# Kernel optimization log

Hardware: AMD Instinct MI355X
Metric: run time of the kernel (lower is better)

## Reference

```python
import jax, jax.numpy as jnp
import numpy as np

LRU_DIM = 256
HIDDEN = 256
H = 64
N = LRU_DIM // H  # 4 (even, per assert)
R_MIN, R_MAX, MAX_PHASE = 0.9, 0.999, 6.28
BSZ, T = 8, 4096


def _rotate_half(x):
    # interleaved pairs: [x0,x1,x2,x3,...] -> [-x1,x0,-x3,x2,...]
    r = jnp.stack([-x[..., 1::2], x[..., 0::2]], axis=-1)
    return r.reshape(x.shape)


def _mix_sequence(gamma, thetas, Us):
    # gamma: scalar, thetas: (N/2,), Us: (T,B,N) -> (T,B,N)
    Tlen = Us.shape[0]
    gammas = jnp.broadcast_to(gamma, (Tlen,))
    ths = jnp.broadcast_to(thetas, (Tlen,) + thetas.shape)

    def binf(a, b):
        gi, ti, xi = a
        gj, tj, xj = b
        theta = jnp.repeat(tj, 2, axis=-1)            # (T, N): [t0,t0,t1,t1,...]
        sin = jnp.sin(theta)[..., None, :]            # (T,1,N)
        cos = jnp.cos(theta)[..., None, :]
        acc = gj[..., None, None] * (cos * xi + sin * _rotate_half(xi)) + xj
        return (gi * gj, ti + tj, acc)

    _, _, res = jax.lax.associative_scan(binf, (gammas, ths, Us), axis=0)
    return res


def setup_inputs() -> dict:
    key = jax.random.key(0)
    ks = jax.random.split(key, 7)
    scale = 1.0 / np.sqrt(HIDDEN + LRU_DIM)
    u = jax.random.normal(ks[0], (BSZ, HIDDEN, T), dtype=jnp.float32)
    thetas_log = jnp.log(jax.random.uniform(ks[1], (H, N // 2), minval=0.01, maxval=1.0) * MAX_PHASE).astype(jnp.float32)
    P_param = (jax.random.normal(ks[2], (H, N, N), dtype=jnp.float32) / np.sqrt(LRU_DIM + N)).astype(jnp.float32)
    B_param = (jax.random.normal(ks[3], (H, N, HIDDEN), dtype=jnp.float32) * scale).astype(jnp.float32)
    C = (jax.random.normal(ks[4], (HIDDEN, LRU_DIM), dtype=jnp.float32) * scale).astype(jnp.float32)
    D = jax.random.normal(ks[5], (HIDDEN,), dtype=jnp.float32)
    u1 = jax.random.uniform(ks[6], (H,))
    gamma_log = (np.log(-np.log(R_MAX)) + u1 * (np.log(-np.log(R_MIN)) - np.log(-np.log(R_MAX)))).astype(jnp.float32)
    return {"u": u, "thetas_log": thetas_log, "P_param": P_param,
            "B_param": B_param, "C": C, "D": D, "gamma_log": gamma_log}


def reference(u, thetas_log, P_param, B_param, C, D, gamma_log):
    Bsz, hidden, Tlen = u.shape
    ut = jnp.transpose(u, (0, 2, 1))                       # (B,T,Dh)
    gamma = jnp.exp(-jnp.exp(gamma_log))                   # (H,)
    trace_per_head = jnp.sum(B_param * B_param, axis=(1, 2))  # tr(B B^T) per head
    norm = jnp.sqrt((1.0 - gamma ** 2) / trace_per_head)
    B_norm = norm[:, None, None] * B_param                 # (H,N,Dh)
    skew = P_param - jnp.swapaxes(P_param, 1, 2)
    P = jax.vmap(jax.scipy.linalg.expm)(skew)              # (H,N,N), orthogonal
    Us = jnp.einsum('HnD,BTD->HTBn', B_norm, ut)           # (H,T,B,N)
    Us = jnp.einsum('HNn,HTBn->HTBN', P, Us)               # == einsum with P^T as in torch
    thetas = jnp.exp(thetas_log)                           # (H,N/2)
    y = jax.vmap(_mix_sequence)(gamma, thetas, Us)         # (H,T,B,N)
    y = jnp.einsum('HNn,HTBN->HTBn', P, y)
    y = jnp.transpose(y, (2, 1, 0, 3)).reshape(Bsz, Tlen, -1)  # (B,T,lru_dim)
    y = jnp.einsum('Dn,BTn->BTD', C, y) + D * ut
    return jnp.transpose(y, (0, 2, 1))                     # (B,Dh,T)
```

## Files before the change

kernel.cpp:

```cpp
#include <hip/hip_runtime.h>
#include <hip/hip_bf16.h>
#include <math.h>


typedef __attribute__((ext_vector_type(8))) short short8;
typedef __attribute__((ext_vector_type(4))) float f32x4;

#define TLEN 4096
#define LCH 64
#define NCH 64
#define BSZ 8
#define LDK 264
#define LDW 132

constexpr int MB_OFF   = 0;
constexpr int CB_OFF   = 32768;
constexpr int AP_OFF   = 65536;
constexpr int ALP_OFF  = AP_OFF + 65 * 256;
constexpr int TOT_OFF  = ALP_OFF + 65 * 256;
constexpr int PL_OFF   = TOT_OFF + NCH * BSZ * 256;
constexpr int NORM_OFF = PL_OFF + 1024;
constexpr int S_OFF    = NORM_OFF + 64;

__device__ __forceinline__ float bfbits2f(unsigned int bits16) {
  union { unsigned int u; float f; } v; v.u = bits16 << 16; return v.f;
}
__device__ __forceinline__ unsigned int f2bfbits(float f) {
  union { float f; unsigned int u; } v; v.f = f;
  return (v.u + 0x7fffu + ((v.u >> 16) & 1u)) >> 16;
}
__device__ __forceinline__ unsigned int pack2(float x, float y) {
  return f2bfbits(x) | (f2bfbits(y) << 16);
}

__global__ __launch_bounds__(256) void k0a_precompute(
    const float* __restrict__ thetas_log, const float* __restrict__ P_param,
    const float* __restrict__ B_param, const float* __restrict__ gamma_log,
    float* __restrict__ ws) {
  __shared__ float tracep[64][4];
  __shared__ double gamma_d[64];
  const int tid = threadIdx.x;
  {
    int h = tid >> 2, q = tid & 3;
    const float* bp = B_param + (h * 4 + q) * 256;
    float s = 0.f;
    for (int i = 0; i < 256; ++i) { float v = bp[i]; s += v * v; }
    tracep[h][q] = s;
  }
  __syncthreads();
  if (tid < 64) {
    int h = tid;
    double g = exp(-exp((double)gamma_log[h]));
    gamma_d[h] = g;
    double tr = (double)tracep[h][0] + tracep[h][1] + tracep[h][2] + tracep[h][3];
    ws[NORM_OFF + h] = (float)sqrt((1.0 - g * g) / tr);
    double A[4][4], E[4][4], Tm[4][4];
    for (int i = 0; i < 4; ++i)
      for (int j = 0; j < 4; ++j)
        A[i][j] = (double)P_param[h * 16 + i * 4 + j] - (double)P_param[h * 16 + j * 4 + i];
    double fro = 0.0;
    for (int i = 0; i < 4; ++i) for (int j = 0; j < 4; ++j) fro += A[i][j] * A[i][j];
    fro = sqrt(fro);
    int s = 0;
    while (fro > 0.25 && s < 30) { fro *= 0.5; ++s; }
    double scl = 1.0;
    for (int q2 = 0; q2 < s; ++q2) scl *= 0.5;
    for (int i = 0; i < 4; ++i) for (int j = 0; j < 4; ++j) A[i][j] *= scl;
    for (int i = 0; i < 4; ++i)
      for (int j = 0; j < 4; ++j) { E[i][j] = (i == j) ? 1.0 : 0.0; Tm[i][j] = E[i][j]; }
    for (int k = 1; k <= 16; ++k) {
      double Tn[4][4];
      for (int i = 0; i < 4; ++i)
        for (int j = 0; j < 4; ++j) {
          double acc = 0.0;
          for (int m = 0; m < 4; ++m) acc += Tm[i][m] * A[m][j];
          Tn[i][j] = acc / (double)k;
        }
      for (int i = 0; i < 4; ++i)
        for (int j = 0; j < 4; ++j) { Tm[i][j] = Tn[i][j]; E[i][j] += Tn[i][j]; }
    }
    for (int q2 = 0; q2 < s; ++q2) {
      double E2[4][4];
      for (int i = 0; i < 4; ++i)
        for (int j = 0; j < 4; ++j) {
          double acc = 0.0;
          for (int m = 0; m < 4; ++m) acc += E[i][m] * E[m][j];
          E2[i][j] = acc;
        }
      for (int i = 0; i < 4; ++i) for (int j = 0; j < 4; ++j) E[i][j] = E2[i][j];
    }
    for (int i = 0; i < 4; ++i)
      for (int j = 0; j < 4; ++j) ws[PL_OFF + h * 16 + i * 4 + j] = (float)E[i][j];
  }
  __syncthreads();
  if (tid < 128) {
    int h = tid >> 1, p = tid & 1;
    double th = exp((double)thetas_log[h * 2 + p]);
    double g = gamma_d[h];
    double ar = g * cos(th), ai = g * sin(th);
    float2* Apw = (float2*)(ws + AP_OFF);
    float2* ALp = (float2*)(ws + ALP_OFF);
    double xr = 1.0, xi = 0.0;
    Apw[tid] = make_float2(1.f, 0.f);
    for (int j = 1; j <= LCH; ++j) {
      double nr = xr * ar - xi * ai, ni = xr * ai + xi * ar;
      xr = nr; xi = ni;
      Apw[j * 128 + tid] = make_float2((float)xr, (float)xi);
    }
    double br = xr, bi = xi;
    xr = 1.0; xi = 0.0;
    ALp[tid] = make_float2(1.f, 0.f);
    for (int k = 1; k <= NCH; ++k) {
      double nr = xr * br - xi * bi, ni = xr * bi + xi * br;
      xr = nr; xi = ni;
      ALp[k * 128 + tid] = make_float2((float)xr, (float)xi);
    }
  }
}

__global__ __launch_bounds__(256) void k0b_mats(
    const float* __restrict__ B_param, const float* __restrict__ C,
    float* __restrict__ ws) {
  const float* Pl  = ws + PL_OFF;
  const float* nrm = ws + NORM_OFF;
  unsigned short* Mbf = (unsigned short*)(ws + MB_OFF);
  unsigned short* Cbf = (unsigned short*)(ws + CB_OFF);
  const int blk = blockIdx.x, tid = threadIdx.x;
  if (blk < 16) {
    for (int rr = 0; rr < 16; ++rr) {
      int r = blk * 16 + rr, h = r >> 2, N = r & 3;
      float acc = 0.f;
      for (int n = 0; n < 4; ++n)
        acc += Pl[h * 16 + N * 4 + n] * B_param[(h * 4 + n) * 256 + tid];
      Mbf[r * 256 + tid] = (unsigned short)f2bfbits(nrm[h] * acc);
    }
  } else {
    int h = tid >> 2;
    int N = tid & 3;
    for (int rr = 0; rr < 16; ++rr) {
      int Do = (blk - 16) * 16 + rr;
      float acc = 0.f;
      for (int n = 0; n < 4; ++n)
        acc += C[Do * 256 + (tid & ~3) + n] * Pl[h * 16 + N * 4 + n];
      Cbf[Do * 256 + tid] = (unsigned short)f2bfbits(acc);
    }
  }
}

__global__ __launch_bounds__(256) void k1_mfma(
    const float* __restrict__ u, float* __restrict__ ws) {
  __shared__ __align__(16) unsigned char smem[64 * LDK * 2];
  unsigned short* us = (unsigned short*)smem;
  unsigned int*   wd = (unsigned int*)smem;

  const int c = blockIdx.x, b = blockIdx.y;
  const int t0 = c * LCH;
  const int tid = threadIdx.x;
  const int L = tid & 63;
  const int w = __builtin_amdgcn_readfirstlane(tid >> 6);
  const int qh = L >> 4, l15 = L & 15;

  {
    const int kbase = tid >> 4;
    const int t4 = (tid & 15) * 4;
#pragma unroll
    for (int i = 0; i < 16; ++i) {
      int d = kbase + i * 16;
      float4 v = *(const float4*)(u + (size_t)(b * 256 + d) * TLEN + t0 + t4);
      float vv[4] = {v.x, v.y, v.z, v.w};
#pragma unroll
      for (int dt = 0; dt < 4; ++dt) {
        int t = t4 + dt;
        us[t * LDK + (d ^ ((t & 3) << 3))] = (unsigned short)f2bfbits(vv[dt]);
      }
    }
  }
  __syncthreads();

  f32x4 acc[4][4];
#pragma unroll
  for (int rt = 0; rt < 4; ++rt)
#pragma unroll
    for (int tt = 0; tt < 4; ++tt) acc[rt][tt] = (f32x4){0.f, 0.f, 0.f, 0.f};
  {
    const unsigned short* Mbf = (const unsigned short*)(ws + MB_OFF);
#pragma unroll
    for (int ks = 0; ks < 8; ++ks) {
      short8 af[4], bf[4];
#pragma unroll
      for (int rt = 0; rt < 4; ++rt)
        af[rt] = *(const short8*)(Mbf + (size_t)(w * 64 + rt * 16 + l15) * 256 + ks * 32 + qh * 8);
#pragma unroll
      for (int tt = 0; tt < 4; ++tt) {
        int row = tt * 16 + l15;
        int col = (ks * 32 + qh * 8) ^ ((row & 3) << 3);
        bf[tt] = *(const short8*)(us + row * LDK + col);
      }
#pragma unroll
      for (int rt = 0; rt < 4; ++rt)
#pragma unroll
        for (int tt = 0; tt < 4; ++tt)
          acc[rt][tt] = __builtin_amdgcn_mfma_f32_16x16x32_bf16(af[rt], bf[tt], acc[rt][tt], 0, 0, 0);
    }
  }
  __syncthreads();

#pragma unroll
  for (int rt = 0; rt < 4; ++rt) {
    int pbase = w * 32 + rt * 8 + qh * 2;
#pragma unroll
    for (int tt = 0; tt < 4; ++tt) {
      int t = tt * 16 + l15;
      f32x4 a4 = acc[rt][tt];
      wd[t * LDW + pbase]     = pack2(a4[0], a4[1]);
      wd[t * LDW + pbase + 1] = pack2(a4[2], a4[3]);
    }
  }
  __syncthreads();

  if (tid < 128) {
    const int p = tid;
    const float2* Apw = (const float2*)(ws + AP_OFF);
    float2 a = Apw[128 + p];
    float zr = 0.f, zi = 0.f;
#pragma unroll
    for (int t = 0; t < LCH; ++t) {
      unsigned int wv = wd[t * LDW + p];
      float wr = bfbits2f(wv & 0xffffu), wi = bfbits2f(wv >> 16);
      float nr = fmaf(a.x, zr, fmaf(-a.y, zi, wr));
      float ni = fmaf(a.x, zi, fmaf(a.y, zr, wi));
      zr = nr; zi = ni;
      wd[t * LDW + p] = pack2(zr, zi);
    }
    ((float2*)(ws + TOT_OFF))[(c * BSZ + b) * 128 + p] = make_float2(zr, zi);
  }
  __syncthreads();

  unsigned int* Sg = (unsigned int*)(ws + S_OFF);
#pragma unroll
  for (int i = 0; i < 32; ++i) {
    int idx = tid + 256 * i;
    int t = idx >> 7, q = idx & 127;
    Sg[(size_t)(t0 + t) * 1024 + b * 128 + q] = wd[t * LDW + q];
  }
}

__global__ __launch_bounds__(256) void k3_mfma(
    const float* __restrict__ u, const float* __restrict__ Dv,
    const float* __restrict__ ws, float* __restrict__ out) {
  __shared__ __align__(16) unsigned char smem[64 * LDK * 2];
  unsigned int* zd = (unsigned int*)smem;

  const int c = blockIdx.x, b = blockIdx.y;
  const int t0 = c * LCH;
  const int tid = threadIdx.x;
  const int L = tid & 63;
  const int w = __builtin_amdgcn_readfirstlane(tid >> 6);
  const int qh = L >> 4, l15 = L & 15;
  const unsigned int* Sg = (const unsigned int*)(ws + S_OFF);

  if (tid < 128) {
    const int p = tid;
    float cr = 0.f, ci = 0.f;
    const float2* ALp = (const float2*)(ws + ALP_OFF);
    const float2* Tot = (const float2*)(ws + TOT_OFF);
    for (int cp = 0; cp < c; ++cp) {
      float2 al = ALp[(c - 1 - cp) * 128 + p];
      float2 tv = Tot[(cp * BSZ + b) * 128 + p];
      cr = fmaf(al.x, tv.x, fmaf(-al.y, tv.y, cr));
      ci = fmaf(al.x, tv.y, fmaf(al.y, tv.x, ci));
    }
    const float2* Apw = (const float2*)(ws + AP_OFF);
#pragma unroll
    for (int t = 0; t < LCH; ++t) {
      unsigned int wv = Sg[(size_t)(t0 + t) * 1024 + b * 128 + p];
      float2 ap = Apw[(t + 1) * 128 + p];
      float sr = fmaf(ap.x, cr, fmaf(-ap.y, ci, bfbits2f(wv & 0xffffu)));
      float si = fmaf(ap.x, ci, fmaf(ap.y, cr, bfbits2f(wv >> 16)));
      zd[t * LDW + p] = pack2(sr, si);
    }
  }
  __syncthreads();

  f32x4 acc[4][4];
#pragma unroll
  for (int rt = 0; rt < 4; ++rt)
#pragma unroll
    for (int tt = 0; tt < 4; ++tt) acc[rt][tt] = (f32x4){0.f, 0.f, 0.f, 0.f};
  {
    const unsigned short* Cbf = (const unsigned short*)(ws + CB_OFF);
    const unsigned short* zs  = (const unsigned short*)smem;
#pragma unroll
    for (int ks = 0; ks < 8; ++ks) {
      short8 af[4], bf[4];
#pragma unroll
      for (int rt = 0; rt < 4; ++rt)
        af[rt] = *(const short8*)(Cbf + (size_t)(w * 64 + rt * 16 + l15) * 256 + ks * 32 + qh * 8);
#pragma unroll
      for (int tt = 0; tt < 4; ++tt)
        bf[tt] = *(const short8*)(zs + (tt * 16 + l15) * LDK + ks * 32 + qh * 8);
#pragma unroll
      for (int rt = 0; rt < 4; ++rt)
#pragma unroll
        for (int tt = 0; tt < 4; ++tt)
          acc[rt][tt] = __builtin_amdgcn_mfma_f32_16x16x32_bf16(af[rt], bf[tt], acc[rt][tt], 0, 0, 0);
    }
  }

  float dv[4][4];
#pragma unroll
  for (int rt = 0; rt < 4; ++rt)
#pragma unroll
    for (int q = 0; q < 4; ++q) dv[rt][q] = Dv[w * 64 + rt * 16 + qh * 4 + q];
#pragma unroll
  for (int rt = 0; rt < 4; ++rt) {
    int Dbase = w * 64 + rt * 16 + qh * 4;
#pragma unroll
    for (int tt = 0; tt < 4; ++tt) {
      int t = tt * 16 + l15;
      f32x4 a4 = acc[rt][tt];
      size_t obase = (size_t)(b * 256 + Dbase) * TLEN + t0 + t;
#pragma unroll
      for (int q = 0; q < 4; ++q)
        out[obase + (size_t)q * TLEN] = a4[q] + dv[rt][q] * u[obase + (size_t)q * TLEN];
    }
  }
}

extern "C" void kernel_launch(void* const* d_in, const int* in_sizes, int n_in,
                              void* d_out, int out_size, void* d_ws, size_t ws_size,
                              hipStream_t stream) {
  const float* u          = (const float*)d_in[0];
  const float* thetas_log = (const float*)d_in[1];
  const float* P_param    = (const float*)d_in[2];
  const float* B_param    = (const float*)d_in[3];
  const float* C          = (const float*)d_in[4];
  const float* Dvec       = (const float*)d_in[5];
  const float* gamma_log  = (const float*)d_in[6];
  float* out = (float*)d_out;
  float* ws  = (float*)d_ws;

  hipLaunchKernelGGL(k0a_precompute, dim3(1), dim3(256), 0, stream,
                     thetas_log, P_param, B_param, gamma_log, ws);
  hipLaunchKernelGGL(k0b_mats, dim3(32), dim3(256), 0, stream, B_param, C, ws);
  hipLaunchKernelGGL(k1_mfma, dim3(NCH, BSZ), dim3(256), 0, stream, u, ws);
  hipLaunchKernelGGL(k3_mfma, dim3(NCH, BSZ), dim3(256), 0, stream, u, Dvec, ws, out);
}
```

Baseline: 169.9 us.

## Recompute chunk states in final kernel instead of storing intermediate scan to global

Restructures the chunked scan so the first pass only emits per-chunk totals and a small sequential kernel computes carries per chunk. The final kernel then recomputes the B projection and the intra-chunk scan from u, seeded with the carry. This removes the global write and read of the full intermediate state and the O(chunks) carry loop each block ran. Chunk length is halved to give more blocks. In exchange the first GEMM runs twice and a serial carry kernel is added. The D*u skip term now uses the bf16-rounded u from shared memory rather than the fp32 input, which loses accuracy.

Result: slower. 188.9 us (+11.2%).

```diff
diff --git a/kernel.cpp b/kernel.cpp
--- a/kernel.cpp
+++ b/kernel.cpp
@@ -7,20 +7,20 @@
 typedef __attribute__((ext_vector_type(4))) float f32x4;
 
 #define TLEN 4096
-#define LCH 64
-#define NCH 64
+#define LCH 32
+#define NCH 128
 #define BSZ 8
 #define LDK 264
 #define LDW 132
 
 constexpr int MB_OFF   = 0;
 constexpr int CB_OFF   = 32768;
-constexpr int AP_OFF   = 65536;
-constexpr int ALP_OFF  = AP_OFF + 65 * 256;
-constexpr int TOT_OFF  = ALP_OFF + 65 * 256;
-constexpr int PL_OFF   = TOT_OFF + NCH * BSZ * 256;
+constexpr int A1_OFF   = 65536;
+constexpr int AL_OFF   = 65792;
+constexpr int TOT_OFF  = 66048;
+constexpr int CAR_OFF  = TOT_OFF + NCH * BSZ * 256;
+constexpr int PL_OFF   = CAR_OFF + NCH * BSZ * 256;
 constexpr int NORM_OFF = PL_OFF + 1024;
-constexpr int S_OFF    = NORM_OFF + 64;
 
 __device__ __forceinline__ float bfbits2f(unsigned int bits16) {
   union { unsigned int u; float f; } v; v.u = bits16 << 16; return v.f;
@@ -98,23 +98,13 @@
     double th = exp((double)thetas_log[h * 2 + p]);
     double g = gamma_d[h];
     double ar = g * cos(th), ai = g * sin(th);
-    float2* Apw = (float2*)(ws + AP_OFF);
-    float2* ALp = (float2*)(ws + ALP_OFF);
-    double xr = 1.0, xi = 0.0;
-    Apw[tid] = make_float2(1.f, 0.f);
-    for (int j = 1; j <= LCH; ++j) {
-      double nr = xr * ar - xi * ai, ni = xr * ai + xi * ar;
+    ((float2*)(ws + A1_OFF))[tid] = make_float2((float)ar, (float)ai);
+    double xr = ar, xi = ai;
+    for (int q = 0; q < 5; ++q) {
+      double nr = xr * xr - xi * xi, ni = 2.0 * xr * xi;
       xr = nr; xi = ni;
-      Apw[j * 128 + tid] = make_float2((float)xr, (float)xi);
-    }
-    double br = xr, bi = xi;
-    xr = 1.0; xi = 0.0;
-    ALp[tid] = make_float2(1.f, 0.f);
-    for (int k = 1; k <= NCH; ++k) {
-      double nr = xr * br - xi * bi, ni = xr * bi + xi * br;
-      xr = nr; xi = ni;
-      ALp[k * 128 + tid] = make_float2((float)xr, (float)xi);
-    }
+    }
+    ((float2*)(ws + AL_OFF))[tid] = make_float2((float)xr, (float)xi);
   }
 }
 
@@ -135,8 +125,7 @@
       Mbf[r * 256 + tid] = (unsigned short)f2bfbits(nrm[h] * acc);
     }
   } else {
-    int h = tid >> 2;
-    int N = tid & 3;
+    int h = tid >> 2, N = tid & 3;
     for (int rr = 0; rr < 16; ++rr) {
       int Do = (blk - 16) * 16 + rr;
       float acc = 0.f;
@@ -147,9 +136,9 @@
   }
 }
 
-__global__ __launch_bounds__(256) void k1_mfma(
+__global__ __launch_bounds__(256) void k1_tot(
     const float* __restrict__ u, float* __restrict__ ws) {
-  __shared__ __align__(16) unsigned char smem[64 * LDK * 2];
+  __shared__ __align__(16) unsigned char smem[LCH * LDK * 2];
   unsigned short* us = (unsigned short*)smem;
   unsigned int*   wd = (unsigned int*)smem;
 
@@ -161,37 +150,34 @@
   const int qh = L >> 4, l15 = L & 15;
 
   {
-    const int kbase = tid >> 4;
-    const int t4 = (tid & 15) * 4;
-#pragma unroll
-    for (int i = 0; i < 16; ++i) {
-      int d = kbase + i * 16;
+    const int kbase = tid >> 3, t4 = (tid & 7) * 4;
+#pragma unroll
+    for (int i = 0; i < 8; ++i) {
+      int d = kbase + i * 32;
       float4 v = *(const float4*)(u + (size_t)(b * 256 + d) * TLEN + t0 + t4);
       float vv[4] = {v.x, v.y, v.z, v.w};
 #pragma unroll
-      for (int dt = 0; dt < 4; ++dt) {
-        int t = t4 + dt;
-        us[t * LDK + (d ^ ((t & 3) << 3))] = (unsigned short)f2bfbits(vv[dt]);
-      }
-    }
-  }
-  __syncthreads();
-
-  f32x4 acc[4][4];
+      for (int dt = 0; dt < 4; ++dt)
+        us[(t4 + dt) * LDK + (d ^ (dt << 3))] = (unsigned short)f2bfbits(vv[dt]);
+    }
+  }
+  __syncthreads();
+
+  f32x4 acc[4][2];
 #pragma unroll
   for (int rt = 0; rt < 4; ++rt)
 #pragma unroll
-    for (int tt = 0; tt < 4; ++tt) acc[rt][tt] = (f32x4){0.f, 0.f, 0.f, 0.f};
+    for (int tt = 0; tt < 2; ++tt) acc[rt][tt] = (f32x4){0.f, 0.f, 0.f, 0.f};
   {
     const unsigned short* Mbf = (const unsigned short*)(ws + MB_OFF);
 #pragma unroll
     for (int ks = 0; ks < 8; ++ks) {
-      short8 af[4], bf[4];
+      short8 af[4], bf[2];
 #pragma unroll
       for (int rt = 0; rt < 4; ++rt)
         af[rt] = *(const short8*)(Mbf + (size_t)(w * 64 + rt * 16 + l15) * 256 + ks * 32 + qh * 8);
 #pragma unroll
-      for (int tt = 0; tt < 4; ++tt) {
+      for (int tt = 0; tt < 2; ++tt) {
         int row = tt * 16 + l15;
         int col = (ks * 32 + qh * 8) ^ ((row & 3) << 3);
         bf[tt] = *(const short8*)(us + row * LDK + col);
@@ -199,7 +185,7 @@
 #pragma unroll
       for (int rt = 0; rt < 4; ++rt)
 #pragma unroll
-        for (int tt = 0; tt < 4; ++tt)
+        for (int tt = 0; tt < 2; ++tt)
           acc[rt][tt] = __builtin_amdgcn_mfma_f32_16x16x32_bf16(af[rt], bf[tt], acc[rt][tt], 0, 0, 0);
     }
   }
@@ -209,20 +195,118 @@
   for (int rt = 0; rt < 4; ++rt) {
     int pbase = w * 32 + rt * 8 + qh * 2;
 #pragma unroll
-    for (int tt = 0; tt < 4; ++tt) {
+    for (int tt = 0; tt < 2; ++tt) {
       int t = tt * 16 + l15;
       f32x4 a4 = acc[rt][tt];
-      wd[t * LDW + pbase]     = pack2(a4[0], a4[1]);
-      wd[t * LDW + pbase + 1] = pack2(a4[2], a4[3]);
+      *(uint2*)&wd[t * LDW + pbase] = make_uint2(pack2(a4[0], a4[1]), pack2(a4[2], a4[3]));
     }
   }
   __syncthreads();
 
   if (tid < 128) {
     const int p = tid;
-    const float2* Apw = (const float2*)(ws + AP_OFF);
-    float2 a = Apw[128 + p];
+    float2 a = ((const float2*)(ws + A1_OFF))[p];
     float zr = 0.f, zi = 0.f;
+#pragma unroll
+    for (int t = 0; t < LCH; ++t) {
+      unsigned int wv = wd[t * LDW + p];
+      float wr = bfbits2f(wv & 0xffffu), wi = bfbits2f(wv >> 16);
+      float nr = fmaf(a.x, zr, fmaf(-a.y, zi, wr));
+      float ni = fmaf(a.x, zi, fmaf(a.y, zr, wi));
+      zr = nr; zi = ni;
+    }
+    ((float2*)(ws + TOT_OFF))[(c * BSZ + b) * 128 + p] = make_float2(zr, zi);
+  }
+}
+
+__global__ __launch_bounds__(128) void k2_carry(float* __restrict__ ws) {
+  const int b = blockIdx.x, p = threadIdx.x;
+  const float2 aL = ((const float2*)(ws + AL_OFF))[p];
+  const float2* Tot = (const float2*)(ws + TOT_OFF);
+  float2* Car = (float2*)(ws + CAR_OFF);
+  float cr = 0.f, ci = 0.f;
+  Car[(0 * BSZ + b) * 128 + p] = make_float2(0.f, 0.f);
+  for (int c = 1; c < NCH; ++c) {
+    float2 tv = Tot[((c - 1) * BSZ + b) * 128 + p];
+    float nr = fmaf(aL.x, cr, fmaf(-aL.y, ci, tv.x));
+    float ni = fmaf(aL.x, ci, fmaf(aL.y, cr, tv.y));
+    cr = nr; ci = ni;
+    Car[(c * BSZ + b) * 128 + p] = make_float2(cr, ci);
+  }
+}
+
+__global__ __launch_bounds__(256) void k3_fused(
+    const float* __restrict__ u, const float* __restrict__ Dv,
+    const float* __restrict__ ws, float* __restrict__ out) {
+  __shared__ __align__(16) unsigned char smem[2 * LCH * LDK * 2];
+  unsigned short* us = (unsigned short*)smem;
+  unsigned int*   wd = (unsigned int*)(smem + LCH * LDK * 2);
+
+  const int c = blockIdx.x, b = blockIdx.y;
+  const int t0 = c * LCH;
+  const int tid = threadIdx.x;
+  const int L = tid & 63;
+  const int w = __builtin_amdgcn_readfirstlane(tid >> 6);
+  const int qh = L >> 4, l15 = L & 15;
+
+  {
+    const int kbase = tid >> 3, t4 = (tid & 7) * 4;
+#pragma unroll
+    for (int i = 0; i < 8; ++i) {
+      int d = kbase + i * 32;
+      float4 v = *(const float4*)(u + (size_t)(b * 256 + d) * TLEN + t0 + t4);
+      float vv[4] = {v.x, v.y, v.z, v.w};
+#pragma unroll
+      for (int dt = 0; dt < 4; ++dt)
+        us[(t4 + dt) * LDK + (d ^ (dt << 3))] = (unsigned short)f2bfbits(vv[dt]);
+    }
+  }
+  __syncthreads();
+
+  f32x4 acc[4][2];
+#pragma unroll
+  for (int rt = 0; rt < 4; ++rt)
+#pragma unroll
+    for (int tt = 0; tt < 2; ++tt) acc[rt][tt] = (f32x4){0.f, 0.f, 0.f, 0.f};
+  {
+    const unsigned short* Mbf = (const unsigned short*)(ws + MB_OFF);
+#pragma unroll
+    for (int ks = 0; ks < 8; ++ks) {
+      short8 af[4], bf[2];
+#pragma unroll
+      for (int rt = 0; rt < 4; ++rt)
+        af[rt] = *(const short8*)(Mbf + (size_t)(w * 64 + rt * 16 + l15) * 256 + ks * 32 + qh * 8);
+#pragma unroll
+      for (int tt = 0; tt < 2; ++tt) {
+        int row = tt * 16 + l15;
+        int col = (ks * 32 + qh * 8) ^ ((row & 3) << 3);
+        bf[tt] = *(const short8*)(us + row * LDK + col);
+      }
+#pragma unroll
+      for (int rt = 0; rt < 4; ++rt)
+#pragma unroll
+        for (int tt = 0; tt < 2; ++tt)
+          acc[rt][tt] = __builtin_amdgcn_mfma_f32_16x16x32_bf16(af[rt], bf[tt], acc[rt][tt], 0, 0, 0);
+    }
+  }
+
+#pragma unroll
+  for (int rt = 0; rt < 4; ++rt) {
+    int pbase = w * 32 + rt * 8 + qh * 2;
+#pragma unroll
+    for (int tt = 0; tt < 2; ++tt) {
+      int t = tt * 16 + l15;
+      f32x4 a4 = acc[rt][tt];
+      *(uint2*)&wd[t * LDW + pbase] = make_uint2(pack2(a4[0], a4[1]), pack2(a4[2], a4[3]));
+    }
+  }
+  __syncthreads();
+
+  if (tid < 128) {
+    const int p = tid;
+    float2 a = ((const float2*)(ws + A1_OFF))[p];
+    float2 cv = ((const float2*)(ws + CAR_OFF))[(c * BSZ + b) * 128 + p];
+    float zr = cv.x, zi = cv.y;
 #pragma unroll
     for (int t = 0; t < LCH; ++t) {
       unsigned int wv = wd[t * LDW + p];
@@ -232,97 +316,49 @@
       zr = nr; zi = ni;
       wd[t * LDW + p] = pack2(zr, zi);
     }
-    ((float2*)(ws + TOT_OFF))[(c * BSZ + b) * 128 + p] = make_float2(zr, zi);
-  }
-  __syncthreads();
-
-  unsigned int* Sg = (unsigned int*)(ws + S_OFF);
-#pragma unroll
-  for (int i = 0; i < 32; ++i) {
-    int idx = tid + 256 * i;
-    int t = idx >> 7, q = idx & 127;
-    Sg[(size_t)(t0 + t) * 1024 + b * 128 + q] = wd[t * LDW + q];
-  }
-}
-
-__global__ __launch_bounds__(256) void k3_mfma(
-    const float* __restrict__ u, const float* __restrict__ Dv,
-    const float* __restrict__ ws, float* __restrict__ out) {
-  __shared__ __align__(16) unsigned char smem[64 * LDK * 2];
-  unsigned int* zd = (unsigned int*)smem;
-
-  const int c = blockIdx.x, b = blockIdx.y;
-  const int t0 = c * LCH;
-  const int tid = threadIdx.x;
-  const int L = tid & 63;
-  const int w = __builtin_amdgcn_readfirstlane(tid >> 6);
-  const int qh = L >> 4, l15 = L & 15;
-  const unsigned int* Sg = (const unsigned int*)(ws + S_OFF);
-
-  if (tid < 128) {
-    const int p = tid;
-    float cr = 0.f, ci = 0.f;
-    const float2* ALp = (const float2*)(ws + ALP_OFF);
-    const float2* Tot = (const float2*)(ws + TOT_OFF);
-    for (int cp = 0; cp < c; ++cp) {
-      float2 al = ALp[(c - 1 - cp) * 128 + p];
-      float2 tv = Tot[(cp * BSZ + b) * 128 + p];
-      cr = fmaf(al.x, tv.x, fmaf(-al.y, tv.y, cr));
-      ci = fmaf(al.x, tv.y, fmaf(al.y, tv.x, ci));
-    }
-    const float2* Apw = (const float2*)(ws + AP_OFF);
-#pragma unroll
-    for (int t = 0; t < LCH; ++t) {
-      unsigned int wv = Sg[(size_t)(t0 + t) * 1024 + b * 128 + p];
-      float2 ap = Apw[(t + 1) * 128 + p];
-      float sr = fmaf(ap.x, cr, fmaf(-ap.y, ci, bfbits2f(wv & 0xffffu)));
-      float si = fmaf(ap.x, ci, fmaf(ap.y, cr, bfbits2f(wv >> 16)));
-      zd[t * LDW + p] = pack2(sr, si);
-    }
-  }
-  __syncthreads();
-
-  f32x4 acc[4][4];
+  }
+  __syncthreads();
+
 #pragma unroll
   for (int rt = 0; rt < 4; ++rt)
 #pragma unroll
-    for (int tt = 0; tt < 4; ++tt) acc[rt][tt] = (f32x4){0.f, 0.f, 0.f, 0.f};
+    for (int tt = 0; tt < 2; ++tt) acc[rt][tt] = (f32x4){0.f, 0.f, 0.f, 0.f};
   {
     const unsigned short* Cbf = (const unsigned short*)(ws + CB_OFF);
-    const unsigned short* zs  = (const unsigned short*)smem;
+    const unsigned short* zs  = (const unsigned short*)wd;
 #pragma unroll
     for (int ks = 0; ks < 8; ++ks) {
-      short8 af[4], bf[4];
+      short8 af[4], bf[2];
 #pragma unroll
       for (int rt = 0; rt < 4; ++rt)
         af[rt] = *(const short8*)(Cbf + (size_t)(w * 64 + rt * 16 + l15) * 256 + ks * 32 + qh * 8);
 #pragma unroll
-      for (int tt = 0; tt < 4; ++tt)
+      for (int tt = 0; tt < 2; ++tt)
         bf[tt] = *(const short8*)(zs + (tt * 16 + l15) * LDK + ks * 32 + qh * 8);
 #pragma unroll
       for (int rt = 0; rt < 4; ++rt)
 #pragma unroll
-        for (int tt = 0; tt < 4; ++tt)
+        for (int tt = 0; tt < 2; ++tt)
           acc[rt][tt] = __builtin_amdgcn_mfma_f32_16x16x32_bf16(af[rt], bf[tt], acc[rt][tt], 0, 0, 0);
     }
   }
 
-  float dv[4][4];
-#pragma unroll
-  for (int rt = 0; rt < 4; ++rt)
-#pragma unroll
-    for (int q = 0; q < 4; ++q) dv[rt][q] = Dv[w * 64 + rt * 16 + qh * 4 + q];
 #pragma unroll
   for (int rt = 0; rt < 4; ++rt) {
     int Dbase = w * 64 + rt * 16 + qh * 4;
-#pragma unroll
-    for (int tt = 0; tt < 4; ++tt) {
+    float dv[4];
+#pragma unroll
+    for (int q = 0; q < 4; ++q) dv[q] = Dv[Dbase + q];
+#pragma unroll
+    for (int tt = 0; tt < 2; ++tt) {
       int t = tt * 16 + l15;
       f32x4 a4 = acc[rt][tt];
       size_t obase = (size_t)(b * 256 + Dbase) * TLEN + t0 + t;
 #pragma unroll
-      for (int q = 0; q < 4; ++q)
-        out[obase + (size_t)q * TLEN] = a4[q] + dv[rt][q] * u[obase + (size_t)q * TLEN];
+      for (int q = 0; q < 4; ++q) {
+        float uu = bfbits2f(us[t * LDK + ((Dbase + q) ^ ((t & 3) << 3))]);
+        out[obase + (size_t)q * TLEN] = a4[q] + dv[q] * uu;
+      }
     }
   }
 }
@@ -343,6 +379,7 @@
   hipLaunchKernelGGL(k0a_precompute, dim3(1), dim3(256), 0, stream,
                      thetas_log, P_param, B_param, gamma_log, ws);
   hipLaunchKernelGGL(k0b_mats, dim3(32), dim3(256), 0, stream, B_param, C, ws);
-  hipLaunchKernelGGL(k1_mfma, dim3(NCH, BSZ), dim3(256), 0, stream, u, ws);
-  hipLaunchKernelGGL(k3_mfma, dim3(NCH, BSZ), dim3(256), 0, stream, u, Dvec, ws, out);
-}
+  hipLaunchKernelGGL(k1_tot, dim3(NCH, BSZ), dim3(256), 0, stream, u, ws);
+  hipLaunchKernelGGL(k2_carry, dim3(BSZ), dim3(128), 0, stream, ws);
+  hipLaunchKernelGGL(k3_fused, dim3(NCH, BSZ), dim3(256), 0, stream, u, Dvec, ws, out);
+}
```
